# Performance work log

Measured on AMD Instinct MI355X. Metric: run time of the kernel, lower is better.

## Reference

```python
import jax, jax.numpy as jnp
import numpy as np

NUM_CLASSES = 10
PIXEL_DIM = 3072  # 3*32*32
N_LAYERS = 3


def setup_inputs() -> dict:
    key = jax.random.key(0)
    k1, k2 = jax.random.split(key)
    x = jax.random.uniform(k1, (512, 3, 32, 32), dtype=jnp.float32)
    # params[c, layer, g] with g = (rz0, ry0, rz1) angles for class-c circuit
    params = jax.random.normal(k2, (NUM_CLASSES, N_LAYERS, 3), dtype=jnp.float32)
    return {"x": x, "params": params}


def _apply_ry(s0, s1, th_half):
    # Ry(t) = [[cos(t/2), -sin(t/2)], [sin(t/2), cos(t/2)]]
    c = jnp.cos(th_half).astype(jnp.complex64)
    s = jnp.sin(th_half).astype(jnp.complex64)
    return c * s0 - s * s1, s * s0 + c * s1


def _apply_rz(s0, s1, th_half):
    # Rz(t) = diag(exp(-i t/2), exp(+i t/2))  (torchquantum convention)
    ph = jnp.exp(-1j * th_half).astype(jnp.complex64)
    return s0 * ph, s1 * jnp.conj(ph)


def reference(x, params):
    B = x.shape[0]
    C = params.shape[0]
    xf = x.reshape(-1)                      # [B*3072] pixel values = Ry encoding angles
    x_half = (0.5 * xf)[None, :]            # broadcast over classes -> [1, N]
    N = xf.shape[0]

    # state |0> per (class, pixel); track the two amplitudes separately
    s0 = jnp.ones((C, N), dtype=jnp.complex64)
    s1 = jnp.zeros((C, N), dtype=jnp.complex64)

    for layer in range(N_LAYERS):
        # data re-uploading: Ry(x)
        s0, s1 = _apply_ry(s0, s1, x_half)
        th = 0.5 * params[:, layer, :]      # [C, 3]
        s0, s1 = _apply_rz(s0, s1, th[:, 0:1])
        s0, s1 = _apply_ry(s0, s1, th[:, 1:2])
        s0, s1 = _apply_rz(s0, s1, th[:, 2:3])

    # MeasureAll(PauliZ): <Z> = |s0|^2 - |s1|^2 ; qout = (<Z>+1)/2 = |s0|^2 (normalized state)
    qout = s0.real ** 2 + s0.imag ** 2      # [C, B*3072]
    return jnp.transpose(qout.reshape(C, B, PIXEL_DIM), (1, 2, 0))  # [B, 3072, C]
```

## Files before the change

### kernel.cpp

```cpp
#include <hip/hip_runtime.h>
#include <math.h>

#define NPIX   (512 * 3072)
#define NCLS   10
#define NLAYER 3
#define PI_4   0.78539816339744830962f

__global__ void coef_kernel(const float* __restrict__ params,
                            float* __restrict__ ws) {
    __shared__ float y[NCLS][8];
    const int t = threadIdx.x;

    if (t < NCLS * 8) {
        const int c = t >> 3;
        const int k = t & 7;
        const float x = (float)k * PI_4;

        float s0r = 1.f, s0i = 0.f, s1r = 0.f, s1i = 0.f;

        #pragma unroll
        for (int l = 0; l < NLAYER; ++l) {
            {
                float sh, ch;
                sincosf(0.5f * x, &sh, &ch);
                float n0r = ch * s0r - sh * s1r;
                float n0i = ch * s0i - sh * s1i;
                float n1r = sh * s0r + ch * s1r;
                float n1i = sh * s0i + ch * s1i;
                s0r = n0r; s0i = n0i; s1r = n1r; s1i = n1i;
            }
            {
                float th = 0.5f * params[(c * NLAYER + l) * 3 + 0];
                float st, ct;
                sincosf(th, &st, &ct);
                float n0r = s0r * ct + s0i * st;
                float n0i = s0i * ct - s0r * st;
                float n1r = s1r * ct - s1i * st;
                float n1i = s1i * ct + s1r * st;
                s0r = n0r; s0i = n0i; s1r = n1r; s1i = n1i;
            }
            {
                float th = 0.5f * params[(c * NLAYER + l) * 3 + 1];
                float sh, ch;
                sincosf(th, &sh, &ch);
                float n0r = ch * s0r - sh * s1r;
                float n0i = ch * s0i - sh * s1i;
                float n1r = sh * s0r + ch * s1r;
                float n1i = sh * s0i + ch * s1i;
                s0r = n0r; s0i = n0i; s1r = n1r; s1i = n1i;
            }
            {
                float th = 0.5f * params[(c * NLAYER + l) * 3 + 2];
                float st, ct;
                sincosf(th, &st, &ct);
                float n0r = s0r * ct + s0i * st;
                float n0i = s0i * ct - s0r * st;
                float n1r = s1r * ct - s1i * st;
                float n1i = s1i * ct + s1r * st;
                s0r = n0r; s0i = n0i; s1r = n1r; s1i = n1i;
            }
        }
        y[c][k] = s0r * s0r + s0i * s0i;
    }

    __syncthreads();

    if (t < NCLS * 7) {
        const int c = t / 7;
        const int j = t % 7;
        float acc = 0.f;
        #pragma unroll
        for (int k = 0; k < 8; ++k) {
            const float ang = (float)k * PI_4;
            float w;
            if (j == 0)       w = 0.125f;
            else if (j <= 3)  w = 0.25f * cosf((float)j * ang);
            else              w = 0.25f * sinf((float)(j - 3) * ang);
            acc += y[c][k] * w;
        }
        ws[c * 7 + j] = acc;
    }
}

__global__ __launch_bounds__(256) void eval_kernel(const float* __restrict__ x,
                                                   const float* __restrict__ coef,
                                                   float* __restrict__ out) {
    __shared__ float lds[256 * 20];

    const int t = threadIdx.x;
    const int g = blockIdx.x * 256 + t;

    const float2 xv = ((const float2* __restrict__)x)[g];
    const float px[2] = {xv.x, xv.y};

    float cf[NCLS * 7];
    #pragma unroll
    for (int i = 0; i < NCLS * 7; ++i) cf[i] = coef[i];

    float r[20];
    #pragma unroll
    for (int p = 0; p < 2; ++p) {
        float s1, c1;
        sincosf(px[p], &s1, &c1);
        const float c2 = 2.f * c1 * c1 - 1.f;
        const float s2 = 2.f * s1 * c1;
        const float c3 = c1 * c2 - s1 * s2;
        const float s3 = s1 * c2 + c1 * s2;
        #pragma unroll
        for (int c = 0; c < NCLS; ++c) {
            const float* f = &cf[c * 7];
            r[p * 10 + c] = f[0] + f[1] * c1 + f[2] * c2 + f[3] * c3
                                 + f[4] * s1 + f[5] * s2 + f[6] * s3;
        }
    }

    float4* wb = (float4*)&lds[t * 20];
    #pragma unroll
    for (int i = 0; i < 5; ++i) wb[i] = ((const float4*)r)[i];

    __syncthreads();

    float4* o4 = (float4*)out + (size_t)blockIdx.x * 1280;
    const float4* l4 = (const float4*)lds;
    #pragma unroll
    for (int i = 0; i < 5; ++i) o4[i * 256 + t] = l4[i * 256 + t];
}

extern "C" void kernel_launch(void* const* d_in, const int* in_sizes, int n_in,
                              void* d_out, int out_size, void* d_ws, size_t ws_size,
                              hipStream_t stream) {
    const float* x      = (const float*)d_in[0];
    const float* params = (const float*)d_in[1];
    float* out          = (float*)d_out;
    float* coef         = (float*)d_ws;

    coef_kernel<<<1, 128, 0, stream>>>(params, coef);

    const int pairs  = NPIX / 2;
    const int blocks = pairs / 256;
    eval_kernel<<<blocks, 256, 0, stream>>>(x, coef, out);
}
```

Baseline: 82.59 us.

## Fuse coefficient computation into eval kernel and use fast sincos

Removes the separate single-block coefficient kernel: every eval block now recomputes the 70 Fourier coefficients from params in shared memory before evaluating its pixels. This removes one launch and the serialization between the two kernels. The cost is that each of the 3072 blocks repeats the small circuit simulation and trig work, adding two extra barriers. It also switches the per-pixel sincos to the fast intrinsic, which is less precise.

```diff
diff --git a/kernel.cpp b/kernel.cpp
--- a/kernel.cpp
+++ b/kernel.cpp
@@ -6,15 +6,22 @@
 #define NLAYER 3
 #define PI_4   0.78539816339744830962f
 
-__global__ void coef_kernel(const float* __restrict__ params,
-                            float* __restrict__ ws) {
-    __shared__ float y[NCLS][8];
+__global__ __launch_bounds__(256) void fused_kernel(const float* __restrict__ x,
+                                                    const float* __restrict__ params,
+                                                    float* __restrict__ out) {
+    __shared__ __align__(16) float y[80];
+    __shared__ __align__(16) float coef[72];
+    __shared__ __align__(16) float tile[5120];
+
     const int t = threadIdx.x;
+    const int g = blockIdx.x * 256 + t;
+
+    const float2 xv = ((const float2* __restrict__)x)[g];
 
     if (t < NCLS * 8) {
         const int c = t >> 3;
         const int k = t & 7;
-        const float x = (float)k * PI_4;
+        const float xs = (float)k * PI_4;
 
         float s0r = 1.f, s0i = 0.f, s1r = 0.f, s1i = 0.f;
 
@@ -22,7 +29,7 @@
         for (int l = 0; l < NLAYER; ++l) {
             {
                 float sh, ch;
-                sincosf(0.5f * x, &sh, &ch);
+                sincosf(0.5f * xs, &sh, &ch);
                 float n0r = ch * s0r - sh * s1r;
                 float n0i = ch * s0i - sh * s1i;
                 float n1r = sh * s0r + ch * s1r;
@@ -60,9 +67,8 @@
                 s0r = n0r; s0i = n0i; s1r = n1r; s1i = n1i;
             }
         }
-        y[c][k] = s0r * s0r + s0i * s0i;
+        y[t] = s0r * s0r + s0i * s0i;
     }
-
     __syncthreads();
 
     if (t < NCLS * 7) {
@@ -76,32 +82,23 @@
             if (j == 0)       w = 0.125f;
             else if (j <= 3)  w = 0.25f * cosf((float)j * ang);
             else              w = 0.25f * sinf((float)(j - 3) * ang);
-            acc += y[c][k] * w;
+            acc += y[c * 8 + k] * w;
         }
-        ws[c * 7 + j] = acc;
+        coef[c * 7 + j] = acc;
     }
-}
+    __syncthreads();
 
-__global__ __launch_bounds__(256) void eval_kernel(const float* __restrict__ x,
-                                                   const float* __restrict__ coef,
-                                                   float* __restrict__ out) {
-    __shared__ float lds[256 * 20];
+    float cf[72];
+    #pragma unroll
+    for (int i = 0; i < 18; ++i)
+        ((float4*)cf)[i] = ((const float4*)coef)[i];
 
-    const int t = threadIdx.x;
-    const int g = blockIdx.x * 256 + t;
-
-    const float2 xv = ((const float2* __restrict__)x)[g];
     const float px[2] = {xv.x, xv.y};
-
-    float cf[NCLS * 7];
-    #pragma unroll
-    for (int i = 0; i < NCLS * 7; ++i) cf[i] = coef[i];
-
     float r[20];
     #pragma unroll
     for (int p = 0; p < 2; ++p) {
         float s1, c1;
-        sincosf(px[p], &s1, &c1);
+        __sincosf(px[p], &s1, &c1);
         const float c2 = 2.f * c1 * c1 - 1.f;
         const float s2 = 2.f * s1 * c1;
         const float c3 = c1 * c2 - s1 * s2;
@@ -114,14 +111,14 @@
         }
     }
 
-    float4* wb = (float4*)&lds[t * 20];
+    float4* wb = (float4*)&tile[t * 20];
     #pragma unroll
     for (int i = 0; i < 5; ++i) wb[i] = ((const float4*)r)[i];
 
     __syncthreads();
 
     float4* o4 = (float4*)out + (size_t)blockIdx.x * 1280;
-    const float4* l4 = (const float4*)lds;
+    const float4* l4 = (const float4*)tile;
     #pragma unroll
     for (int i = 0; i < 5; ++i) o4[i * 256 + t] = l4[i * 256 + t];
 }
@@ -132,11 +129,9 @@
     const float* x      = (const float*)d_in[0];
     const float* params = (const float*)d_in[1];
     float* out          = (float*)d_out;
-    float* coef         = (float*)d_ws;
-
-    coef_kernel<<<1, 128, 0, stream>>>(params, coef);
+    (void)d_ws; (void)ws_size;
 
     const int pairs  = NPIX / 2;
     const int blocks = pairs / 256;
-    eval_kernel<<<blocks, 256, 0, stream>>>(x, coef, out);
+    fused_kernel<<<blocks, 256, 0, stream>>>(x, params, out);
 }
```

Measured after the change: 87.82 us. 1.06x slower.
